# Kernel tuning notes

Measured on AMD Instinct MI355X. Metric: run time of the kernel, lower is better.

The kernel has to match this reference:

```python
import jax, jax.numpy as jnp
import numpy as np

DIM = 384
EPS = 1e-12  # F.normalize default eps


def setup_inputs() -> dict:
    key = jax.random.key(0)
    ks = jax.random.split(key, 6)
    b, c, h, w = 4, DIM, 64, 64
    x = jax.random.normal(ks[0], (b, c, h, w), dtype=jnp.float32)
    gamma = jnp.ones((c,), dtype=jnp.float32)  # WanRMS_norm gamma, init ones
    # 1x1 convs are per-pixel linear maps: [out_c, in_c] weight + bias
    w_qkv = jax.random.normal(ks[1], (3 * c, c), dtype=jnp.float32) * (1.0 / np.sqrt(c))
    b_qkv = jax.random.normal(ks[2], (3 * c,), dtype=jnp.float32) * 0.01
    w_proj = jax.random.normal(ks[3], (c, c), dtype=jnp.float32) * (1.0 / np.sqrt(c))
    b_proj = jax.random.normal(ks[4], (c,), dtype=jnp.float32) * 0.01
    return {"x": x, "gamma": gamma, "w_qkv": w_qkv, "b_qkv": b_qkv,
            "w_proj": w_proj, "b_proj": b_proj}


def reference(x, gamma, w_qkv, b_qkv, w_proj, b_proj):
    b, c, h, w = x.shape
    identity = x
    # WanRMS_norm: F.normalize over channel dim * sqrt(dim) * gamma
    l2 = jnp.sqrt(jnp.sum(x * x, axis=1, keepdims=True))
    xn = x / jnp.maximum(l2, EPS) * jnp.sqrt(jnp.float32(c)) * gamma[None, :, None, None]
    # 1x1 conv qkv: [b, 3c, h, w]
    qkv = jnp.einsum("bchw,oc->bohw", xn, w_qkv) + b_qkv[None, :, None, None]
    # flatten spatial -> tokens: [b, 3c, s] -> q/k/v each [b, s, c]
    s = h * w
    qkv = qkv.reshape(b, 3 * c, s).transpose(0, 2, 1)  # [b, s, 3c]
    q, k, v = jnp.split(qkv, 3, axis=-1)
    # single-head scaled dot-product attention (non-causal, as in Wan SDPA call)
    scores = jnp.einsum("bqc,bkc->bqk", q, k) / jnp.sqrt(jnp.float32(c))
    attn = jax.nn.softmax(scores, axis=-1)
    out = jnp.einsum("bqk,bkc->bqc", attn, v)  # [b, s, c]
    out = out.transpose(0, 2, 1).reshape(b, c, h, w)
    # 1x1 proj conv + residual
    out = jnp.einsum("bchw,oc->bohw", out, w_proj) + b_proj[None, :, None, None]
    return out + identity
```

## Files before the change

### kernel.cpp

```cpp
#include <hip/hip_runtime.h>
#include <cstdint>
#include <cstddef>

typedef __bf16 bf16;
typedef __bf16 bf16x8 __attribute__((ext_vector_type(8)));
typedef float  f32x4 __attribute__((ext_vector_type(4)));
typedef float  f32x16 __attribute__((ext_vector_type(16)));
typedef int    i32x4 __attribute__((ext_vector_type(4)));
typedef int    i32x8 __attribute__((ext_vector_type(8)));

#define MFMA16(a, b, c) __builtin_amdgcn_mfma_f32_16x16x32_bf16((a), (b), (c), 0, 0, 0)
#define MFMA_MX(a, b, c) \
    __builtin_amdgcn_mfma_scale_f32_32x32x64_f8f6f4((a), (b), (c), 0, 0, 0, 0x7F, 0, 0x7F)

#if __has_builtin(__builtin_amdgcn_exp2f)
#define EXP2(x) __builtin_amdgcn_exp2f(x)
#else
#define EXP2(x) exp2f(x)
#endif

__device__ __forceinline__ uint8_t to_fp8(float v) {
    return (uint8_t)(__builtin_amdgcn_cvt_pk_fp8_f32(v, v, 0, false) & 0xff);
}

__device__ __forceinline__ i32x8 ld32(const void* p) {
    i32x4 a = *(const i32x4*)p;
    i32x4 b = *(const i32x4*)((const char*)p + 16);
    i32x8 r;
    r[0] = a[0]; r[1] = a[1]; r[2] = a[2]; r[3] = a[3];
    r[4] = b[0]; r[5] = b[1]; r[6] = b[2]; r[7] = b[3];
    return r;
}

__device__ __forceinline__ void gload16(const void* g, void* l) {
    __builtin_amdgcn_global_load_lds(
        (const __attribute__((address_space(1))) unsigned int*)g,
        (__attribute__((address_space(3))) unsigned int*)l,
        16, 0, 0);
}

__global__ __launch_bounds__(256) void norm_kernel(
    const float* __restrict__ x, const float* __restrict__ gamma,
    const float* __restrict__ wqkv, const float* __restrict__ wproj,
    bf16* __restrict__ xn, bf16* __restrict__ wq, bf16* __restrict__ wp)
{
    const int tid = threadIdx.x;
    const int blk = blockIdx.x;
    if (blk >= 256) {
        int t0 = (blk - 256) * 256 + tid;
        for (int t = t0; t < 1152 * 384 + 384 * 384; t += 128 * 256) {
            if (t < 1152 * 384) wq[t] = (bf16)wqkv[t];
            else                wp[t - 1152 * 384] = (bf16)wproj[t - 1152 * 384];
        }
        return;
    }
    __shared__ float sG[384];
    __shared__ float sS[4][64];
    __shared__ float sScale[64];
    const int w = tid >> 6, l = tid & 63;
    for (int i = tid; i < 384; i += 256) sG[i] = gamma[i];
    const int b = blk >> 6, p0 = (blk & 63) << 6;
    const float* xb = x + ((size_t)b * 384) * 4096 + p0 + l;
    const float* xc = xb + (size_t)(96 * w) * 4096;
    float s0 = 0.f, s1 = 0.f;
#pragma unroll 8
    for (int c = 0; c < 96; c += 2) {
        float v0 = xc[(size_t)c * 4096];
        float v1 = xc[(size_t)(c + 1) * 4096];
        s0 += v0 * v0; s1 += v1 * v1;
    }
    sS[w][l] = s0 + s1;
    __syncthreads();
    if (w == 0) {
        float t = (sS[0][l] + sS[1][l]) + (sS[2][l] + sS[3][l]);
        sScale[l] = 19.595917942265423f / fmaxf(sqrtf(t), 1e-12f);
    }
    __syncthreads();
    float sc = sScale[l];
    int tok = (b << 12) + p0 + l;
    bf16* o = xn + (size_t)tok * 384 + 96 * w;
    for (int c0 = 0; c0 < 96; c0 += 8) {
        bf16x8 v8;
#pragma unroll
        for (int j = 0; j < 8; ++j)
            v8[j] = (bf16)(xc[(size_t)(c0 + j) * 4096] * sc * sG[96 * w + c0 + j]);
        *(bf16x8*)(o + c0) = v8;
    }
}

__device__ __forceinline__ void gemm_core_bt(
    bf16* sA, bf16* sB,
    const bf16* __restrict__ A, const bf16* __restrict__ B,
    const float* __restrict__ bias_m, const float* __restrict__ bias_n,
    uint8_t* __restrict__ Cout, const int mode, const int ldc,
    const int m0, const int n0)
{
    const int tid = threadIdx.x;
    const int l = tid & 63, w = tid >> 6;
    const int lo = l & 15, hi = l >> 4;
    const int wm = w >> 1, wn = w & 1;

    f32x4 acc[4][4] = {};

    for (int kt = 0; kt < 6; ++kt) {
        __syncthreads();
        const int k0 = kt * 64;
#pragma unroll
        for (int i = 0; i < 5; ++i) {
            int ci = i * 256 + tid;
            if (ci < 1152) {
                int row = ci / 9, off = ci % 9;
                gload16(A + (size_t)(m0 + row) * 384 + k0 + off * 8, (char*)sA + ci * 16);
                gload16(B + (size_t)(n0 + row) * 384 + k0 + off * 8, (char*)sB + ci * 16);
            }
        }
        __syncthreads();
#pragma unroll
        for (int ks = 0; ks < 2; ++ks) {
            bf16x8 af[4], bfr[4];
#pragma unroll
            for (int t = 0; t < 4; ++t)
                af[t] = *(const bf16x8*)(sA + (wm * 64 + t * 16 + lo) * 72 + ks * 32 + hi * 8);
#pragma unroll
            for (int t = 0; t < 4; ++t)
                bfr[t] = *(const bf16x8*)(sB + (wn * 64 + t * 16 + lo) * 72 + ks * 32 + hi * 8);
#pragma unroll
            for (int rt = 0; rt < 4; ++rt)
#pragma unroll
                for (int ct = 0; ct < 4; ++ct)
                    acc[rt][ct] = MFMA16(af[rt], bfr[ct], acc[rt][ct]);
        }
    }

#pragma unroll
    for (int rt = 0; rt < 4; ++rt) {
#pragma unroll
        for (int ct = 0; ct < 4; ++ct) {
            int mb = m0 + wm * 64 + rt * 16 + hi * 4;
            int n  = n0 + wn * 64 + ct * 16 + lo;
            if (mode == 0) {
                float bn = bias_n[n];
#pragma unroll
                for (int r = 0; r < 4; ++r)
                    Cout[(size_t)(mb + r) * ldc + n] = to_fp8(acc[rt][ct][r] + bn);
            } else {
#pragma unroll
                for (int r = 0; r < 4; ++r)
                    Cout[(size_t)(mb + r) * ldc + n] = to_fp8(acc[rt][ct][r] + bias_m[mb + r]);
            }
        }
    }
}

__global__ __launch_bounds__(256) void gemm_qkv(
    const bf16* __restrict__ xn, const bf16* __restrict__ wq,
    const float* __restrict__ b_qkv, uint8_t* __restrict__ qkb,
    uint8_t* __restrict__ vtb)
{
    __shared__ bf16 sA[128 * 72];
    __shared__ bf16 sB[128 * 72];
    const int id = blockIdx.x;
    if (id < 768) {
        const int xcd = id & 7, s = id >> 3;
        gemm_core_bt(sA, sB, xn, wq, nullptr, b_qkv, qkb, 0, 768,
                     (xcd * 16 + s / 6) * 128, (s % 6) * 128);
    } else {
        const int t = id - 768;
        const int xcd = t & 7, s = t >> 3;
        gemm_core_bt(sA, sB, wq + (size_t)768 * 384, xn, b_qkv + 768, nullptr,
                     vtb, 1, 16384, (s % 3) * 128, (xcd * 16 + s / 3) * 128);
    }
}

__global__ __launch_bounds__(256) void gemm_proj(
    const bf16* __restrict__ wp, const bf16* __restrict__ p0,
    const bf16* __restrict__ p1, const float* __restrict__ ml,
    const float* __restrict__ b_proj, const float* __restrict__ x,
    float* __restrict__ out)
{
    __shared__ bf16 sA[128 * 72];
    __shared__ bf16 sB[128 * 72];
    const int tid = threadIdx.x;
    const int l = tid & 63, w = tid >> 6;
    const int lo = l & 15, hi = l >> 4;
    const int wm = w >> 1, wn = w & 1;
    const int id = blockIdx.x;
    const int xcd = id & 7, s = id >> 3;
    const int m0 = (s % 3) * 128, n0 = (xcd * 16 + s / 3) * 128;

    f32x4 acc[4][4] = {};

    for (int kt = 0; kt < 6; ++kt) {
        __syncthreads();
        const int k0 = kt * 64;
#pragma unroll
        for (int i = 0; i < 5; ++i) {
            int ci = i * 256 + tid;
            if (ci < 1152) {
                int row = ci / 9, off = ci % 9;
                gload16(wp + (size_t)(m0 + row) * 384 + k0 + off * 8, (char*)sA + ci * 16);
                int tok = n0 + row;
                float2 ml0 = *(const float2*)(ml + (size_t)tok * 2);
                float2 ml1 = *(const float2*)(ml + (size_t)(16384 + tok) * 2);
                float mM = fmaxf(ml0.x, ml1.x);
                float a0 = EXP2(ml0.x - mM), a1 = EXP2(ml1.x - mM);
                float inv = 1.0f / (a0 * ml0.y + a1 * ml1.y);
                float w0 = a0 * inv, w1 = a1 * inv;
                size_t boff = (size_t)tok * 384 + k0 + off * 8;
                bf16x8 v0 = *(const bf16x8*)(p0 + boff);
                bf16x8 v1 = *(const bf16x8*)(p1 + boff);
                bf16x8 r;
#pragma unroll
                for (int j = 0; j < 8; ++j)
                    r[j] = (bf16)((float)v0[j] * w0 + (float)v1[j] * w1);
                *(bf16x8*)((char*)sB + ci * 16) = r;
            }
        }
        __syncthreads();
#pragma unroll
        for (int ks = 0; ks < 2; ++ks) {
            bf16x8 af[4], bfr[4];
#pragma unroll
            for (int t = 0; t < 4; ++t)
                af[t] = *(const bf16x8*)(sA + (wm * 64 + t * 16 + lo) * 72 + ks * 32 + hi * 8);
#pragma unroll
            for (int t = 0; t < 4; ++t)
                bfr[t] = *(const bf16x8*)(sB + (wn * 64 + t * 16 + lo) * 72 + ks * 32 + hi * 8);
#pragma unroll
            for (int rt = 0; rt < 4; ++rt)
#pragma unroll
                for (int ct = 0; ct < 4; ++ct)
                    acc[rt][ct] = MFMA16(af[rt], bfr[ct], acc[rt][ct]);
        }
    }

#pragma unroll
    for (int rt = 0; rt < 4; ++rt) {
#pragma unroll
        for (int ct = 0; ct < 4; ++ct) {
            int mb = m0 + wm * 64 + rt * 16 + hi * 4;
            int n  = n0 + wn * 64 + ct * 16 + lo;
            int bb = n >> 12, p = n & 4095;
#pragma unroll
            for (int r = 0; r < 4; ++r) {
                int m = mb + r;
                size_t idx = ((size_t)(bb * 384 + m)) * 4096 + p;
                out[idx] = acc[rt][ct][r] + b_proj[m] + x[idx];
            }
        }
    }
}

__device__ __forceinline__ void stage_K64(
    const uint8_t* __restrict__ qk, int kv0, uint8_t* dstK, int tid)
{
    const uint8_t* kb = qk + (size_t)kv0 * 768 + 384;
#pragma unroll
    for (int i = 0; i < 7; ++i) {
        int ci = i * 256 + tid;
        if (ci < 1600) {
            int row = ci / 25, off = ci % 25;
            gload16(kb + (size_t)row * 768 + off * 16, dstK + ci * 16);
        }
    }
}

__device__ __forceinline__ void stage_V64(
    const uint8_t* __restrict__ vt, int kv0, uint8_t* sV, int tid)
{
    const uint8_t* vb = vt + kv0;
#pragma unroll
    for (int i = 0; i < 8; ++i) {
        int ci = i * 256 + tid;
        if (ci < 1920) {
            int row = ci / 5, off = ci % 5;
            gload16(vb + (size_t)row * 16384 + off * 16, sV + ci * 16);
        }
    }
}

__global__ __launch_bounds__(256, 2) void flash_kernel(
    const uint8_t* __restrict__ qk, const uint8_t* __restrict__ vt,
    bf16* __restrict__ op0, bf16* __restrict__ op1, float* __restrict__ ml)
{
    extern __shared__ char smem[];
    uint8_t* sbase = (uint8_t*)smem;
    uint8_t* sV = sbase + 51200;
    const int tid = threadIdx.x;
    const int l = tid & 63, w = tid >> 6;
    const int l31 = l & 31, hi2 = l >> 5;
    const int wq = w >> 1, wd = w & 1;
    const int id = blockIdx.x;
    const int qt = id >> 3, bh = id & 7;
    const int b = bh >> 1, half = bh & 1;
    const int q0 = b * 4096 + qt * 64;
    const int kvbase = b * 4096 + half * 2048;
    const float SC = 0.07362217057594547f;
    const float THR = 108.664f;

    stage_K64(qk, kvbase, sbase, tid);

    i32x8 qf[6];
    {
        const uint8_t* qrow = qk + (size_t)(q0 + wq * 32 + l31) * 768 + hi2 * 32;
#pragma unroll
        for (int ksw = 0; ksw < 6; ++ksw)
            qf[ksw] = ld32(qrow + ksw * 64);
    }

    f32x16 o[6] = {};
    float m = -1e30f, lsum = 0.f;

    __syncthreads();

    int c = 0;
    for (int kt = 0; kt < 32; ++kt) {
        stage_V64(vt, kvbase + kt * 64, sV, tid);
        if (kt < 31) stage_K64(qk, kvbase + (kt + 1) * 64, sbase + (c ^ 1) * 25600, tid);

        uint8_t* sK = sbase + c * 25600;
        f32x16 s0 = {}, s1 = {};
        __builtin_amdgcn_s_setprio(1);
#pragma unroll
        for (int ksw = 0; ksw < 6; ++ksw) {
            i32x8 ak0 = ld32(sK + (size_t)l31 * 400 + ksw * 64 + hi2 * 32);
            i32x8 ak1 = ld32(sK + (size_t)(32 + l31) * 400 + ksw * 64 + hi2 * 32);
            s0 = MFMA_MX(ak0, qf[ksw], s0);
            s1 = MFMA_MX(ak1, qf[ksw], s1);
        }
        __builtin_amdgcn_s_setprio(0);

        float a0 = fmaxf(fmaxf(s0[0],  s0[1]),  fmaxf(s0[2],  s0[3]));
        float a1 = fmaxf(fmaxf(s0[4],  s0[5]),  fmaxf(s0[6],  s0[7]));
        float a2 = fmaxf(fmaxf(s0[8],  s0[9]),  fmaxf(s0[10], s0[11]));
        float a3 = fmaxf(fmaxf(s0[12], s0[13]), fmaxf(s0[14], s0[15]));
        float b0 = fmaxf(fmaxf(s1[0],  s1[1]),  fmaxf(s1[2],  s1[3]));
        float b1 = fmaxf(fmaxf(s1[4],  s1[5]),  fmaxf(s1[6],  s1[7]));
        float b2 = fmaxf(fmaxf(s1[8],  s1[9]),  fmaxf(s1[10], s1[11]));
        float b3 = fmaxf(fmaxf(s1[12], s1[13]), fmaxf(s1[14], s1[15]));
        float mx = fmaxf(fmaxf(fmaxf(a0, a1), fmaxf(a2, a3)),
                         fmaxf(fmaxf(b0, b1), fmaxf(b2, b3)));
        mx = fmaxf(mx, __shfl_xor(mx, 32));
        if (__any(mx > m + THR)) {
            float mn = fmaxf(m, mx);
            float alpha = EXP2((m - mn) * SC);
            m = mn;
            lsum *= alpha;
#pragma unroll
            for (int dt = 0; dt < 6; ++dt)
#pragma unroll
                for (int r = 0; r < 16; ++r) o[dt][r] *= alpha;
        }
        float p0[16], p1[16];
        float msc = m * SC;
        float rsa = 0.f, rsb = 0.f, rsc = 0.f, rsd = 0.f;
#pragma unroll
        for (int r = 0; r < 16; r += 4) {
            p0[r]     = EXP2(fmaf(s0[r],     SC, -msc)); rsa += p0[r];
            p0[r + 1] = EXP2(fmaf(s0[r + 1], SC, -msc)); rsb += p0[r + 1];
            p0[r + 2] = EXP2(fmaf(s0[r + 2], SC, -msc)); rsc += p0[r + 2];
            p0[r + 3] = EXP2(fmaf(s0[r + 3], SC, -msc)); rsd += p0[r + 3];
        }
#pragma unroll
        for (int r = 0; r < 16; r += 4) {
            p1[r]     = EXP2(fmaf(s1[r],     SC, -msc)); rsa += p1[r];
            p1[r + 1] = EXP2(fmaf(s1[r + 1], SC, -msc)); rsb += p1[r + 1];
            p1[r + 2] = EXP2(fmaf(s1[r + 2], SC, -msc)); rsc += p1[r + 2];
            p1[r + 3] = EXP2(fmaf(s1[r + 3], SC, -msc)); rsd += p1[r + 3];
        }
        float rs = (rsa + rsb) + (rsc + rsd);
        rs += __shfl_xor(rs, 32);
        lsum += rs;

        int pk0[4], pk1[4];
#pragma unroll
        for (int i = 0; i < 4; ++i) {
            int d = __builtin_amdgcn_cvt_pk_fp8_f32(p0[4 * i], p0[4 * i + 1], 0, false);
            pk0[i] = __builtin_amdgcn_cvt_pk_fp8_f32(p0[4 * i + 2], p0[4 * i + 3], d, true);
            d = __builtin_amdgcn_cvt_pk_fp8_f32(p1[4 * i], p1[4 * i + 1], 0, false);
            pk1[i] = __builtin_amdgcn_cvt_pk_fp8_f32(p1[4 * i + 2], p1[4 * i + 3], d, true);
        }
        i32x8 pf;
#pragma unroll
        for (int i = 0; i < 4; ++i) {
            int x0 = __shfl_xor(pk0[i], 32);
            int x1 = __shfl_xor(pk1[i], 32);
            int own = hi2 ? pk1[i] : pk0[i];
            int oth = hi2 ? x1 : x0;
            pf[2 * i]     = hi2 ? oth : own;
            pf[2 * i + 1] = hi2 ? own : oth;
        }

        __syncthreads();

        __builtin_amdgcn_s_setprio(1);
#pragma unroll
        for (int dt = 0; dt < 6; ++dt) {
            i32x8 av = ld32(sV + (size_t)(wd * 192 + dt * 32 + l31) * 80 + hi2 * 32);
            o[dt] = MFMA_MX(av, pf, o[dt]);
        }
        __builtin_amdgcn_s_setprio(0);

        __syncthreads();
        c ^= 1;
    }

    float* tr = (float*)(smem + w * 4608);
    bf16* dst = half ? op1 : op0;
#pragma unroll
    for (int dt = 0; dt < 6; ++dt) {
#pragma unroll
        for (int r = 0; r < 16; ++r) {
            int d32 = (r & 3) + 8 * (r >> 2) + 4 * hi2;
            tr[l31 * 36 + d32] = o[dt][r];
        }
        f32x4 v0 = *(f32x4*)(tr + l31 * 36 + hi2 * 16 + 0);
        f32x4 v1 = *(f32x4*)(tr + l31 * 36 + hi2 * 16 + 4);
        f32x4 v2 = *(f32x4*)(tr + l31 * 36 + hi2 * 16 + 8);
        f32x4 v3 = *(f32x4*)(tr + l31 * 36 + hi2 * 16 + 12);
        bf16x8 h0, h1;
#pragma unroll
        for (int j = 0; j < 4; ++j) {
            h0[j] = (bf16)v0[j]; h0[4 + j] = (bf16)v1[j];
            h1[j] = (bf16)v2[j]; h1[4 + j] = (bf16)v3[j];
        }
        size_t tok = (size_t)(q0 + wq * 32 + l31);
        bf16* drow = dst + tok * 384 + wd * 192 + dt * 32 + hi2 * 16;
        *(bf16x8*)(drow + 0) = h0;
        *(bf16x8*)(drow + 8) = h1;
        __syncthreads();
    }
    if (wd == 0 && hi2 == 0) {
        int tok = q0 + wq * 32 + l31;
        ml[(size_t)(half * 16384 + tok) * 2 + 0] = m * SC;
        ml[(size_t)(half * 16384 + tok) * 2 + 1] = lsum;
    }
}

extern "C" void kernel_launch(void* const* d_in, const int* in_sizes, int n_in,
                              void* d_out, int out_size, void* d_ws, size_t ws_size,
                              hipStream_t stream) {
    const float* x      = (const float*)d_in[0];
    const float* gamma  = (const float*)d_in[1];
    const float* w_qkv  = (const float*)d_in[2];
    const float* b_qkv  = (const float*)d_in[3];
    const float* w_proj = (const float*)d_in[4];
    const float* b_proj = (const float*)d_in[5];
    float* out = (float*)d_out;

    char* ws = (char*)d_ws;
    bf16* xn  = (bf16*)ws;    ws += (size_t)16384 * 384 * 2;
    uint8_t* qkb = (uint8_t*)ws; ws += (size_t)16384 * 768;
    uint8_t* vtb = (uint8_t*)ws; ws += (size_t)384 * 16384;
    bf16* ob  = (bf16*)ws;    ws += (size_t)16384 * 384 * 2;
    bf16* wqb = (bf16*)ws;    ws += (size_t)1152 * 384 * 2;
    bf16* wpb = (bf16*)ws;    ws += (size_t)384 * 384 * 2;
    float* mlb = (float*)ws;  ws += (size_t)2 * 16384 * 2 * 4;

    (void)hipFuncSetAttribute((const void*)flash_kernel,
                              hipFuncAttributeMaxDynamicSharedMemorySize, 81920);

    norm_kernel<<<384, 256, 0, stream>>>(x, gamma, w_qkv, w_proj, xn, wqb, wpb);
    gemm_qkv<<<1152, 256, 0, stream>>>(xn, wqb, b_qkv, qkb, vtb);
    flash_kernel<<<512, 256, 81920, stream>>>(qkb, vtb, xn, ob, mlb);
    gemm_proj<<<384, 256, 0, stream>>>(wpb, xn, ob, mlb, b_proj, x, out);
}
```

Before: 252.7 us.

## Load V tiles straight to registers and drop the LDS V staging

The attention kernel now reads each 64-token V slice directly from global memory into registers, rather than copying it into shared memory and reading it back. This removes the barrier between the softmax and PV phases and the per-chunk barriers in the epilogue, and shrinks dynamic shared memory from 81920 to 51200 bytes. K staging offsets are precomputed once per block and then advanced by a fixed stride each tile, which removes per-tile divide and modulo work. In exchange, each lane keeps six extra 32-byte V fragments live, which raises register pressure. The two query-row waves that share a V half now fetch the same data separately, so more global and L2 traffic goes through the vector memory path.

```diff
diff --git a/kernel.cpp b/kernel.cpp
--- a/kernel.cpp
+++ b/kernel.cpp
@@ -251,41 +251,12 @@
     }
 }
 
-__device__ __forceinline__ void stage_K64(
-    const uint8_t* __restrict__ qk, int kv0, uint8_t* dstK, int tid)
-{
-    const uint8_t* kb = qk + (size_t)kv0 * 768 + 384;
-#pragma unroll
-    for (int i = 0; i < 7; ++i) {
-        int ci = i * 256 + tid;
-        if (ci < 1600) {
-            int row = ci / 25, off = ci % 25;
-            gload16(kb + (size_t)row * 768 + off * 16, dstK + ci * 16);
-        }
-    }
-}
-
-__device__ __forceinline__ void stage_V64(
-    const uint8_t* __restrict__ vt, int kv0, uint8_t* sV, int tid)
-{
-    const uint8_t* vb = vt + kv0;
-#pragma unroll
-    for (int i = 0; i < 8; ++i) {
-        int ci = i * 256 + tid;
-        if (ci < 1920) {
-            int row = ci / 5, off = ci % 5;
-            gload16(vb + (size_t)row * 16384 + off * 16, sV + ci * 16);
-        }
-    }
-}
-
 __global__ __launch_bounds__(256, 2) void flash_kernel(
     const uint8_t* __restrict__ qk, const uint8_t* __restrict__ vt,
     bf16* __restrict__ op0, bf16* __restrict__ op1, float* __restrict__ ml)
 {
     extern __shared__ char smem[];
     uint8_t* sbase = (uint8_t*)smem;
-    uint8_t* sV = sbase + 51200;
     const int tid = threadIdx.x;
     const int l = tid & 63, w = tid >> 6;
     const int l31 = l & 31, hi2 = l >> 5;
@@ -298,7 +269,23 @@
     const float SC = 0.07362217057594547f;
     const float THR = 108.664f;
 
-    stage_K64(qk, kvbase, sbase, tid);
+    uint32_t ksrc[7];
+#pragma unroll
+    for (int i = 0; i < 7; ++i) {
+        int ci = i * 256 + tid;
+        int row = ci / 25, off = ci % 25;
+        ksrc[i] = (uint32_t)((kvbase + row) * 768 + 384 + off * 16);
+    }
+#pragma unroll
+    for (int i = 0; i < 7; ++i) {
+        if (i < 6 || tid < 64) gload16(qk + ksrc[i], sbase + i * 4096 + tid * 16);
+        ksrc[i] += 49152;
+    }
+
+    uint32_t voff[6];
+#pragma unroll
+    for (int dt = 0; dt < 6; ++dt)
+        voff[dt] = (uint32_t)((wd * 192 + dt * 32 + l31) * 16384 + kvbase + hi2 * 32);
 
     i32x8 qf[6];
     {
@@ -315,10 +302,22 @@
 
     int c = 0;
     for (int kt = 0; kt < 32; ++kt) {
-        stage_V64(vt, kvbase + kt * 64, sV, tid);
-        if (kt < 31) stage_K64(qk, kvbase + (kt + 1) * 64, sbase + (c ^ 1) * 25600, tid);
-
-        uint8_t* sK = sbase + c * 25600;
+        if (kt < 31) {
+            uint8_t* dst = sbase + (c ^ 1) * 25600;
+#pragma unroll
+            for (int i = 0; i < 7; ++i) {
+                if (i < 6 || tid < 64) gload16(qk + ksrc[i], dst + i * 4096 + tid * 16);
+                ksrc[i] += 49152;
+            }
+        }
+        i32x8 av[6];
+#pragma unroll
+        for (int dt = 0; dt < 6; ++dt) {
+            av[dt] = ld32(vt + voff[dt]);
+            voff[dt] += 64;
+        }
+
+        const uint8_t* sK = sbase + c * 25600;
         f32x16 s0 = {}, s1 = {};
         __builtin_amdgcn_s_setprio(1);
 #pragma unroll
@@ -391,14 +390,10 @@
             pf[2 * i + 1] = hi2 ? own : oth;
         }
 
-        __syncthreads();
-
         __builtin_amdgcn_s_setprio(1);
 #pragma unroll
-        for (int dt = 0; dt < 6; ++dt) {
-            i32x8 av = ld32(sV + (size_t)(wd * 192 + dt * 32 + l31) * 80 + hi2 * 32);
-            o[dt] = MFMA_MX(av, pf, o[dt]);
-        }
+        for (int dt = 0; dt < 6; ++dt)
+            o[dt] = MFMA_MX(av[dt], pf, o[dt]);
         __builtin_amdgcn_s_setprio(0);
 
         __syncthreads();
@@ -428,7 +423,6 @@
         bf16* drow = dst + tok * 384 + wd * 192 + dt * 32 + hi2 * 16;
         *(bf16x8*)(drow + 0) = h0;
         *(bf16x8*)(drow + 8) = h1;
-        __syncthreads();
     }
     if (wd == 0 && hi2 == 0) {
         int tok = q0 + wq * 32 + l31;
@@ -458,10 +452,10 @@
     float* mlb = (float*)ws;  ws += (size_t)2 * 16384 * 2 * 4;
 
     (void)hipFuncSetAttribute((const void*)flash_kernel,
-                              hipFuncAttributeMaxDynamicSharedMemorySize, 81920);
+                              hipFuncAttributeMaxDynamicSharedMemorySize, 51200);
 
     norm_kernel<<<384, 256, 0, stream>>>(x, gamma, w_qkv, w_proj, xn, wqb, wpb);
     gemm_qkv<<<1152, 256, 0, stream>>>(xn, wqb, b_qkv, qkb, vtb);
-    flash_kernel<<<512, 256, 81920, stream>>>(qkb, vtb, xn, ob, mlb);
+    flash_kernel<<<512, 256, 51200, stream>>>(qkb, vtb, xn, ob, mlb);
     gemm_proj<<<384, 256, 0, stream>>>(wpb, xn, ob, mlb, b_proj, x, out);
 }
```

Measured after the change: 289.9 us. 14.7% more time.
